# Performance work log

Measured on AMD Instinct MI355X. Metric: run time of the kernel, lower is better.

The kernel has to match this reference:

```python
import jax, jax.numpy as jnp
import numpy as np

B, R, L, F, H = 65536, 12, 16, 8, 64  # batch, rss_dim, n_leds, led_feat_dim, head_dim

def setup_inputs() -> dict:
    key = jax.random.key(0)
    ks = jax.random.split(key, 20)
    p = lambda k, shp, s=0.1: (jax.random.normal(k, shp, dtype=jnp.float32) * s)
    return {
        "rss_t": jax.random.uniform(ks[0], (B, R, 1), dtype=jnp.float32),
        "led_features": jax.random.normal(ks[1], (B, L, F), dtype=jnp.float32),
        "led_positions": jax.random.normal(ks[2], (B, L, 3), dtype=jnp.float32),
        "prev_pos": jax.random.normal(ks[3], (B, 3), dtype=jnp.float32),
        "freq_mask": jax.random.randint(ks[4], (R, L), 0, 2).astype(jnp.int32),
        # intensity_gate: Linear(1,16) -> ReLU -> Linear(16,1) -> Sigmoid
        "gw1": p(ks[5], (1, 16)), "gb1": p(ks[6], (16,)),
        "gw2": p(ks[7], (16, 1)), "gb2": p(ks[8], (1,)),
        # query_proj: Linear(1,32) -> ReLU -> Linear(32,64)
        "qw1": p(ks[9], (1, 32)), "qb1": p(ks[10], (32,)),
        "qw2": p(ks[11], (32, H)), "qb2": p(ks[12], (H,)),
        # key_proj: Linear(F+3,32) -> ReLU -> Linear(32,64)
        "kw1": p(ks[13], (F + 3, 32)), "kb1": p(ks[14], (32,)),
        "kw2": p(ks[15], (32, H)), "kb2": p(ks[16], (H,)),
        "sigma": jnp.float32(0.5),
    }

def reference(rss_t, led_features, led_positions, prev_pos, freq_mask,
              gw1, gb1, gw2, gb2, qw1, qb1, qw2, qb2, kw1, kb1, kw2, kb2, sigma):
    # intensity gate with hard threshold
    gate = jax.nn.sigmoid(jax.nn.relu(rss_t @ gw1 + gb1) @ gw2 + gb2)  # [B,R,1]
    iw = (rss_t > 0.5).astype(rss_t.dtype) * gate                      # [B,R,1]
    # query / key projections
    Q = jax.nn.relu((rss_t * iw) @ qw1 + qb1) @ qw2 + qb2              # [B,R,H]
    led_input = jnp.concatenate([led_features, led_positions], axis=-1)  # [B,L,F+3]
    K = jax.nn.relu(led_input @ kw1 + kb1) @ kw2 + kb2                 # [B,L,H]
    scores = jnp.einsum("brh,blh->brl", Q, K)                          # [B,R,L]
    # distance bias
    dist_sq = jnp.sum((prev_pos[:, None, :] - led_positions) ** 2, axis=-1)  # [B,L]
    scores = scores - dist_sq[:, None, :] / (2.0 * sigma ** 2)
    # mask + softmax
    neg = jnp.finfo(scores.dtype).min
    scores = jnp.where(freq_mask[None, :, :] == 0, neg, scores)
    attn = jax.nn.softmax(scores, axis=-1)                             # [B,R,L]
    return attn, iw.squeeze(-1)
```

## Files before the change

### kernel.cpp

```cpp
#include <hip/hip_runtime.h>

#define B_TOT 65536
#define R 12
#define L 16
#define NB 8
#define NEG_MIN -3.402823466e38f

#define WS_V   0
#define WS_C   32
#define WS_PM  40
#define WS_BP  64
#define WS_TAB 96
#define TROW   72
#define WS_WF  2472

#define WROWS (4 * 16 * 40 + 8)

typedef __attribute__((ext_vector_type(8))) short short8;
typedef __attribute__((ext_vector_type(4))) float f32x4;

static __device__ __forceinline__ short f2bf(float f) {
    uint32_t u = __float_as_uint(f);
    uint32_t r = u + 0x7FFFu + ((u >> 16) & 1u);
    return (short)(r >> 16);
}

static __device__ __forceinline__ unsigned cvt_pk_bf16(float a, float b) {
    unsigned d;
    asm("v_cvt_pk_bf16_f32 %0, %1, %2" : "=v"(d) : "v"(a), "v"(b));
    return d;
}

__global__ __launch_bounds__(256) void nfh_pre(
    const float* __restrict__ qw1, const float* __restrict__ qb1,
    const float* __restrict__ qw2, const float* __restrict__ qb2,
    const float* __restrict__ kw2, const float* __restrict__ kb2,
    const float* __restrict__ kw1, const float* __restrict__ kb1,
    const int*   __restrict__ fmask,
    float* __restrict__ ws)
{
    __shared__ float sM[1024];
    __shared__ float su[32];
    __shared__ float sw1[32], sb1[32], sbp[32], sbq[32];
    const int t = threadIdx.x;

    if (t < 32) { sw1[t] = qw1[t]; sb1[t] = qb1[t]; }
    for (int e = t; e < 1024; e += 256) {
        const int i = e >> 5, j = e & 31;
        float acc = 0.f;
        for (int h = 0; h < 64; ++h) acc = fmaf(qw2[i * 64 + h], kw2[j * 64 + h], acc);
        sM[e] = acc;
    }
    if (t < 32) {
        float au = 0.f, av = 0.f;
        for (int h = 0; h < 64; ++h) {
            au = fmaf(qw2[t * 64 + h], kb2[h], au);
            av = fmaf(kw2[t * 64 + h], qb2[h], av);
        }
        su[t] = au;
        ws[WS_V + t] = av;
        const float w = qw1[t];
        sbp[t] = (w != 0.f) ? (-qb1[t] / w) : 3.0e30f;
    }
    if (t == 64) {
        float acc = 0.f;
        for (int h = 0; h < 64; ++h) acc = fmaf(qb2[h], kb2[h], acc);
        ws[WS_C] = acc;
    }
    if (t < 12) {
        int pm = 0;
        for (int l = 0; l < 16; ++l) if (fmask[t * 16 + l] != 0) pm |= (1 << l);
        ((int*)ws)[WS_PM + t] = pm;
    }
    __syncthreads();
    if (t < 32) {
        const float key = sbp[t];
        int rank = 0;
        #pragma unroll
        for (int i = 0; i < 32; ++i) {
            const float vi = sbp[i];
            rank += (vi < key || (vi == key && i < t)) ? 1 : 0;
        }
        sbq[rank] = key;
    }
    __syncthreads();
    if (t < 32) ws[WS_BP + t] = sbq[t];

    for (int task = t; task < 33 * 32 + 33; task += 256) {
        const int m = (task < 33 * 32) ? (task >> 5) : (task - 33 * 32);
        const float xi = (m == 0) ? sbq[0] - 1.f
                       : ((m == 32) ? sbq[31] + 1.f
                                    : sbq[m - 1] + 0.5f * (sbq[m] - sbq[m - 1]));
        if (task < 33 * 32) {
            const int j = task & 31;
            float A = 0.f, Bv = 0.f;
            for (int i = 0; i < 32; ++i) {
                if (fmaf(sw1[i], xi, sb1[i]) > 0.f) {
                    A  = fmaf(sw1[i], sM[i * 32 + j], A);
                    Bv = fmaf(sb1[i], sM[i * 32 + j], Bv);
                }
            }
            ws[WS_TAB + m * TROW + j] = A;
            ws[WS_TAB + m * TROW + 36 + j] = Bv;
        } else {
            float Au = 0.f, Bu = 0.f;
            for (int i = 0; i < 32; ++i) {
                if (fmaf(sw1[i], xi, sb1[i]) > 0.f) {
                    Au = fmaf(sw1[i], su[i], Au);
                    Bu = fmaf(sb1[i], su[i], Bu);
                }
            }
            ws[WS_TAB + m * TROW + 32] = Au;
            ws[WS_TAB + m * TROW + 36 + 32] = Bu;
        }
    }

    {
        const int fr = t >> 6;
        const int li = t & 63;
        const int jl = li & 15, kb = li >> 4;
        const int T = fr & 1, term = fr >> 1;
        const int q = ((jl >> 2) << 3) + (T << 2) + (jl & 3);
        short* wsp = (short*)(ws + WS_WF);
        #pragma unroll
        for (int e = 0; e < 8; ++e) {
            const int k = kb * 8 + e;
            float w = 0.f;
            if (term == 0) {
                if (k < 11)       w = kw1[k * 32 + q];
                else if (k == 11) w = kb1[q];
            } else {
                if (k < 11)       w = kw1[k * 32 + q];
                else if (k == 11) { const float b = kb1[q];
                                    w = b - __uint_as_float(((uint32_t)(uint16_t)f2bf(b)) << 16); }
                else if (k < 23)  { const float a = kw1[(k - 12) * 32 + q];
                                    w = a - __uint_as_float(((uint32_t)(uint16_t)f2bf(a)) << 16); }
            }
            wsp[(fr * 64 + li) * 8 + e] = f2bf(w);
        }
    }
}

__global__ __launch_bounds__(128, 4) void nfh_main(
    const float* __restrict__ rss,
    const float* __restrict__ feat,
    const float* __restrict__ pos,
    const float* __restrict__ prev,
    const float* __restrict__ gw1, const float* __restrict__ gb1,
    const float* __restrict__ gw2, const float* __restrict__ gb2,
    const float* __restrict__ sigma_p,
    const float* __restrict__ ws,
    float* __restrict__ out)
{
    __shared__ short s_in[2 * WROWS];
    __shared__ short s_ttf[NB * 384];
    __shared__ float s_dq[NB * 16];
    __shared__ float s_tc[NB * 12];

    const int t = threadIdx.x;
    const int lane = t & 63;
    const int wv = t >> 6;
    const int lg = lane >> 4;
    const int b0 = blockIdx.x * NB;
    const float sigma = sigma_p[0];
    const float inv2s2 = 1.f / (2.f * sigma * sigma);

    const short* wsp = (const short*)(ws + WS_WF);
    const short8 wf0 = *(const short8*)(wsp + (0 * 64 + lane) * 8);
    const short8 wf1 = *(const short8*)(wsp + (1 * 64 + lane) * 8);
    const short8 wf2 = *(const short8*)(wsp + (2 * 64 + lane) * 8);
    const short8 wf3 = *(const short8*)(wsp + (3 * 64 + lane) * 8);
    const f32x4 v0 = *(const f32x4*)(ws + WS_V + lg * 8);
    const f32x4 v1 = *(const f32x4*)(ws + WS_V + lg * 8 + 4);
    const float cconst = ws[WS_C];

    if (lane < 8) s_in[wv * WROWS + 4 * 16 * 40 + lane] = 0;

    {
        const int bb1 = t >> 4, l1 = t & 15;
        const int b = b0 + bb1;
        float in[12];
        const float4* f4 = (const float4*)(feat + ((size_t)b * (L * 8) + l1 * 8));
        const float4 fa = f4[0], fb = f4[1];
        in[0] = fa.x; in[1] = fa.y; in[2] = fa.z; in[3] = fa.w;
        in[4] = fb.x; in[5] = fb.y; in[6] = fb.z; in[7] = fb.w;
        const float* pp = pos + ((size_t)b * (L * 3) + l1 * 3);
        in[8] = pp[0]; in[9] = pp[1]; in[10] = pp[2];
        in[11] = 1.0f;

        float dsq = 0.f;
        #pragma unroll
        for (int m = 0; m < 3; ++m) {
            const float d = prev[b * 3 + m] - in[8 + m];
            dsq = fmaf(d, d, dsq);
        }
        s_dq[bb1 * 16 + l1] = cconst - dsq * inv2s2;

        unsigned hp[6], lp[6];
        #pragma unroll
        for (int p = 0; p < 6; ++p) {
            const float a = in[2 * p], c = in[2 * p + 1];
            const unsigned h = cvt_pk_bf16(a, c);
            hp[p] = h;
            const float h0 = __uint_as_float(h << 16);
            const float h1 = __uint_as_float(h & 0xFFFF0000u);
            lp[p] = cvt_pk_bf16(a - h0, c - h1);
        }
        const unsigned lp5m = (lp[5] & 0xFFFFu) | 0x3F800000u;

        uint4* rowp = (uint4*)&s_in[wv * WROWS + ((bb1 & 3) * 16 + l1) * 40];
        rowp[0] = make_uint4(hp[0], hp[1], hp[2], hp[3]);
        rowp[1] = make_uint4(hp[4], hp[5], 0u, 0u);
        rowp[2] = make_uint4(lp[0], lp[1], lp[2], lp[3]);
        rowp[3] = make_uint4(lp[4], lp5m, hp[0], hp[1]);
        rowp[4] = make_uint4(hp[2], hp[3], hp[4], hp[5] & 0xFFFFu);
    }

    if ((t & 15) < R) {
        const int bb2 = t >> 4;
        const int r2 = t & 15;
        const int b = b0 + bb2;
        const float x = rss[(size_t)b * R + r2];
        float z = gb2[0];
        #pragma unroll
        for (int i = 0; i < 16; ++i) {
            const float h = fmaxf(fmaf(x, gw1[i], gb1[i]), 0.f);
            z = fmaf(h, gw2[i], z);
        }
        const float gate = 1.f / (1.f + __expf(-z));
        const float iw = (x > 0.5f) ? gate : 0.f;
        out[(size_t)B_TOT * R * L + (size_t)b * R + r2] = iw;
        const float xq = x * iw;

        int k = 0;
        #pragma unroll
        for (int m = 0; m < 32; ++m) k += (xq > ws[WS_BP + m]) ? 1 : 0;
        const float* row = ws + WS_TAB + k * TROW;
        const float4* ra = (const float4*)row;
        const float4* rb = (const float4*)(row + 36);
        s_tc[bb2 * 12 + r2] = fmaf(xq, row[32], row[68]);
        #pragma unroll
        for (int kb = 0; kb < 4; ++kb) {
            const float4 a0 = ra[kb * 2], c0 = rb[kb * 2];
            const float4 a1 = ra[kb * 2 + 1], c1 = rb[kb * 2 + 1];
            uint4 pk;
            pk.x = cvt_pk_bf16(fmaf(xq, a0.x, c0.x), fmaf(xq, a0.y, c0.y));
            pk.y = cvt_pk_bf16(fmaf(xq, a0.z, c0.z), fmaf(xq, a0.w, c0.w));
            pk.z = cvt_pk_bf16(fmaf(xq, a1.x, c1.x), fmaf(xq, a1.y, c1.y));
            pk.w = cvt_pk_bf16(fmaf(xq, a1.z, c1.z), fmaf(xq, a1.w, c1.w));
            *(uint4*)&s_ttf[bb2 * 384 + (kb * 12 + r2) * 8] = pk;
        }
    }

    asm volatile("s_waitcnt lgkmcnt(0)" ::: "memory");

    {
        const int r = lane & 15;
        const int pm = (r < R) ? ((const int*)ws)[WS_PM + r] : 0;

        #pragma unroll
        for (int i = 0; i < 4; ++i) {
            const int bb = wv * 4 + i;
            const short* rowb = &s_in[wv * WROWS + (i * 16 + r) * 40];
            const short8 i1 = *(const short8*)(rowb + lg * 8);
            const short8 i2 = *(const short8*)(rowb + 16 + lg * 8);

            f32x4 d0 = {0.f, 0.f, 0.f, 0.f};
            f32x4 d1 = {0.f, 0.f, 0.f, 0.f};
            d0 = __builtin_amdgcn_mfma_f32_16x16x32_bf16(wf0, i1, d0, 0, 0, 0);
            d0 = __builtin_amdgcn_mfma_f32_16x16x32_bf16(wf2, i2, d0, 0, 0, 0);
            d1 = __builtin_amdgcn_mfma_f32_16x16x32_bf16(wf1, i1, d1, 0, 0, 0);
            d1 = __builtin_amdgcn_mfma_f32_16x16x32_bf16(wf3, i2, d1, 0, 0, 0);

            float vbp = 0.f;
            #pragma unroll
            for (int j = 0; j < 4; ++j) {
                d0[j] = fmaxf(d0[j], 0.f);
                vbp = fmaf(v0[j], d0[j], vbp);
            }
            #pragma unroll
            for (int j = 0; j < 4; ++j) {
                d1[j] = fmaxf(d1[j], 0.f);
                vbp = fmaf(v1[j], d1[j], vbp);
            }
            vbp += __shfl_xor(vbp, 16);
            vbp += __shfl_xor(vbp, 32);
            const float vbl = vbp + s_dq[bb * 16 + r];

            uint4 afp;
            afp.x = cvt_pk_bf16(d0[0], d0[1]);
            afp.y = cvt_pk_bf16(d0[2], d0[3]);
            afp.z = cvt_pk_bf16(d1[0], d1[1]);
            afp.w = cvt_pk_bf16(d1[2], d1[3]);
            const short8 af = *(const short8*)&afp;

            short8 bf = (short8){0, 0, 0, 0, 0, 0, 0, 0};
            float tc = 0.f;
            if (r < R) {
                bf = *(const short8*)&s_ttf[bb * 384 + (lg * 12 + r) * 8];
                tc = s_tc[bb * 12 + r];
            }
            f32x4 acc = {0.f, 0.f, 0.f, 0.f};
            acc = __builtin_amdgcn_mfma_f32_16x16x32_bf16(af, bf, acc, 0, 0, 0);

            float sc[4];
            #pragma unroll
            for (int j = 0; j < 4; ++j) {
                const float vbj = __shfl(vbl, lg * 4 + j);
                sc[j] = acc[j] + tc + vbj;
                if (!((pm >> (lg * 4 + j)) & 1)) sc[j] = NEG_MIN;
            }
            float mx = fmaxf(fmaxf(sc[0], sc[1]), fmaxf(sc[2], sc[3]));
            mx = fmaxf(mx, __shfl_xor(mx, 16));
            mx = fmaxf(mx, __shfl_xor(mx, 32));
            float sum = 0.f;
            #pragma unroll
            for (int j = 0; j < 4; ++j) { sc[j] = __expf(sc[j] - mx); sum += sc[j]; }
            sum += __shfl_xor(sum, 16);
            sum += __shfl_xor(sum, 32);
            const float inv = 1.f / sum;

            if (r < R) {
                float4* op = (float4*)(out + ((size_t)(b0 + bb) * R + r) * L + lg * 4);
                *op = make_float4(sc[0] * inv, sc[1] * inv, sc[2] * inv, sc[3] * inv);
            }
        }
    }
}

extern "C" void kernel_launch(void* const* d_in, const int* in_sizes, int n_in,
                              void* d_out, int out_size, void* d_ws, size_t ws_size,
                              hipStream_t stream) {
    const float* rss   = (const float*)d_in[0];
    const float* feat  = (const float*)d_in[1];
    const float* pos   = (const float*)d_in[2];
    const float* prev  = (const float*)d_in[3];
    const int*   fmask = (const int*)d_in[4];
    const float* gw1   = (const float*)d_in[5];
    const float* gb1   = (const float*)d_in[6];
    const float* gw2   = (const float*)d_in[7];
    const float* gb2   = (const float*)d_in[8];
    const float* qw1   = (const float*)d_in[9];
    const float* qb1   = (const float*)d_in[10];
    const float* qw2   = (const float*)d_in[11];
    const float* qb2   = (const float*)d_in[12];
    const float* kw1   = (const float*)d_in[13];
    const float* kb1   = (const float*)d_in[14];
    const float* kw2   = (const float*)d_in[15];
    const float* kb2   = (const float*)d_in[16];
    const float* sigma = (const float*)d_in[17];
    float* out = (float*)d_out;
    float* ws  = (float*)d_ws;

    nfh_pre<<<1, 256, 0, stream>>>(qw1, qb1, qw2, qb2, kw2, kb2, kw1, kb1, fmask, ws);
    nfh_main<<<B_TOT / NB, 128, 0, stream>>>(
        rss, feat, pos, prev,
        gw1, gb1, gw2, gb2,
        sigma, ws, out);
}
```

Measured before the change: 172.0 us.

## Build query tables per lane via shuffles, drop shared staging, double block size

```diff
diff --git a/kernel.cpp b/kernel.cpp
--- a/kernel.cpp
+++ b/kernel.cpp
@@ -3,7 +3,7 @@
 #define B_TOT 65536
 #define R 12
 #define L 16
-#define NB 8
+#define NB 16
 #define NEG_MIN -3.402823466e38f
 
 #define WS_V   0
@@ -141,7 +141,7 @@
     }
 }
 
-__global__ __launch_bounds__(128, 4) void nfh_main(
+__global__ __launch_bounds__(256, 8) void nfh_main(
     const float* __restrict__ rss,
     const float* __restrict__ feat,
     const float* __restrict__ pos,
@@ -152,10 +152,7 @@
     const float* __restrict__ ws,
     float* __restrict__ out)
 {
-    __shared__ short s_in[2 * WROWS];
-    __shared__ short s_ttf[NB * 384];
-    __shared__ float s_dq[NB * 16];
-    __shared__ float s_tc[NB * 12];
+    __shared__ short s_in[4 * WROWS];
 
     const int t = threadIdx.x;
     const int lane = t & 63;
@@ -176,6 +173,7 @@
 
     if (lane < 8) s_in[wv * WROWS + 4 * 16 * 40 + lane] = 0;
 
+    float my_dq;
     {
         const int bb1 = t >> 4, l1 = t & 15;
         const int b = b0 + bb1;
@@ -194,7 +192,7 @@
             const float d = prev[b * 3 + m] - in[8 + m];
             dsq = fmaf(d, d, dsq);
         }
-        s_dq[bb1 * 16 + l1] = cconst - dsq * inv2s2;
+        my_dq = cconst - dsq * inv2s2;
 
         unsigned hp[6], lp[6];
         #pragma unroll
@@ -216,54 +214,50 @@
         rowp[4] = make_uint4(hp[2], hp[3], hp[4], hp[5] & 0xFFFFu);
     }
 
-    if ((t & 15) < R) {
+    float my_xq = 0.f;
+    {
         const int bb2 = t >> 4;
         const int r2 = t & 15;
-        const int b = b0 + bb2;
-        const float x = rss[(size_t)b * R + r2];
-        float z = gb2[0];
-        #pragma unroll
-        for (int i = 0; i < 16; ++i) {
-            const float h = fmaxf(fmaf(x, gw1[i], gb1[i]), 0.f);
-            z = fmaf(h, gw2[i], z);
-        }
-        const float gate = 1.f / (1.f + __expf(-z));
-        const float iw = (x > 0.5f) ? gate : 0.f;
-        out[(size_t)B_TOT * R * L + (size_t)b * R + r2] = iw;
-        const float xq = x * iw;
-
-        int k = 0;
-        #pragma unroll
-        for (int m = 0; m < 32; ++m) k += (xq > ws[WS_BP + m]) ? 1 : 0;
-        const float* row = ws + WS_TAB + k * TROW;
-        const float4* ra = (const float4*)row;
-        const float4* rb = (const float4*)(row + 36);
-        s_tc[bb2 * 12 + r2] = fmaf(xq, row[32], row[68]);
-        #pragma unroll
-        for (int kb = 0; kb < 4; ++kb) {
-            const float4 a0 = ra[kb * 2], c0 = rb[kb * 2];
-            const float4 a1 = ra[kb * 2 + 1], c1 = rb[kb * 2 + 1];
-            uint4 pk;
-            pk.x = cvt_pk_bf16(fmaf(xq, a0.x, c0.x), fmaf(xq, a0.y, c0.y));
-            pk.y = cvt_pk_bf16(fmaf(xq, a0.z, c0.z), fmaf(xq, a0.w, c0.w));
-            pk.z = cvt_pk_bf16(fmaf(xq, a1.x, c1.x), fmaf(xq, a1.y, c1.y));
-            pk.w = cvt_pk_bf16(fmaf(xq, a1.z, c1.z), fmaf(xq, a1.w, c1.w));
-            *(uint4*)&s_ttf[bb2 * 384 + (kb * 12 + r2) * 8] = pk;
-        }
-    }
+        if (r2 < R) {
+            const int b = b0 + bb2;
+            const float x = rss[(size_t)b * R + r2];
+            float z = gb2[0];
+            #pragma unroll
+            for (int i = 0; i < 16; ++i) {
+                const float h = fmaxf(fmaf(x, gw1[i], gb1[i]), 0.f);
+                z = fmaf(h, gw2[i], z);
+            }
+            const float gate = 1.f / (1.f + __expf(-z));
+            const float iw = (x > 0.5f) ? gate : 0.f;
+            out[(size_t)B_TOT * R * L + (size_t)b * R + r2] = iw;
+            my_xq = x * iw;
+        }
+    }
+    int my_k = 0;
+    #pragma unroll
+    for (int m = 0; m < 32; ++m) my_k += (my_xq > ws[WS_BP + m]) ? 1 : 0;
+    const float* myrow = ws + WS_TAB + my_k * TROW;
+    const float my_tc = fmaf(my_xq, myrow[32], myrow[68]);
 
     asm volatile("s_waitcnt lgkmcnt(0)" ::: "memory");
 
     {
         const int r = lane & 15;
         const int pm = (r < R) ? ((const int*)ws)[WS_PM + r] : 0;
-
-        #pragma unroll
+        const int j0 = lg * 8;
+
+        #pragma unroll 1
         for (int i = 0; i < 4; ++i) {
             const int bb = wv * 4 + i;
+            const int src = i * 16 + r;
+            const float xq_s = __shfl(my_xq, src);
+            const int   k_s  = __shfl(my_k,  src);
+            const float tc_s = __shfl(my_tc, src);
+            const float dq_s = __shfl(my_dq, src);
+
             const short* rowb = &s_in[wv * WROWS + (i * 16 + r) * 40];
-            const short8 i1 = *(const short8*)(rowb + lg * 8);
-            const short8 i2 = *(const short8*)(rowb + 16 + lg * 8);
+            const short8 i1 = *(const short8*)(rowb + j0);
+            const short8 i2 = *(const short8*)(rowb + 16 + j0);
 
             f32x4 d0 = {0.f, 0.f, 0.f, 0.f};
             f32x4 d1 = {0.f, 0.f, 0.f, 0.f};
@@ -285,7 +279,7 @@
             }
             vbp += __shfl_xor(vbp, 16);
             vbp += __shfl_xor(vbp, 32);
-            const float vbl = vbp + s_dq[bb * 16 + r];
+            const float vbl = vbp + dq_s;
 
             uint4 afp;
             afp.x = cvt_pk_bf16(d0[0], d0[1]);
@@ -294,12 +288,18 @@
             afp.w = cvt_pk_bf16(d1[2], d1[3]);
             const short8 af = *(const short8*)&afp;
 
-            short8 bf = (short8){0, 0, 0, 0, 0, 0, 0, 0};
-            float tc = 0.f;
-            if (r < R) {
-                bf = *(const short8*)&s_ttf[bb * 384 + (lg * 12 + r) * 8];
-                tc = s_tc[bb * 12 + r];
-            }
+            const float* rowt = ws + WS_TAB + k_s * TROW;
+            const float4 a0 = *(const float4*)(rowt + j0);
+            const float4 a1 = *(const float4*)(rowt + j0 + 4);
+            const float4 c0 = *(const float4*)(rowt + 36 + j0);
+            const float4 c1 = *(const float4*)(rowt + 36 + j0 + 4);
+            uint4 bfp;
+            bfp.x = cvt_pk_bf16(fmaf(xq_s, a0.x, c0.x), fmaf(xq_s, a0.y, c0.y));
+            bfp.y = cvt_pk_bf16(fmaf(xq_s, a0.z, c0.z), fmaf(xq_s, a0.w, c0.w));
+            bfp.z = cvt_pk_bf16(fmaf(xq_s, a1.x, c1.x), fmaf(xq_s, a1.y, c1.y));
+            bfp.w = cvt_pk_bf16(fmaf(xq_s, a1.z, c1.z), fmaf(xq_s, a1.w, c1.w));
+            const short8 bf = *(const short8*)&bfp;
+
             f32x4 acc = {0.f, 0.f, 0.f, 0.f};
             acc = __builtin_amdgcn_mfma_f32_16x16x32_bf16(af, bf, acc, 0, 0, 0);
 
@@ -307,7 +307,7 @@
             #pragma unroll
             for (int j = 0; j < 4; ++j) {
                 const float vbj = __shfl(vbl, lg * 4 + j);
-                sc[j] = acc[j] + tc + vbj;
+                sc[j] = acc[j] + tc_s + vbj;
                 if (!((pm >> (lg * 4 + j)) & 1)) sc[j] = NEG_MIN;
             }
             float mx = fmaxf(fmaxf(sc[0], sc[1]), fmaxf(sc[2], sc[3]));
@@ -353,7 +353,7 @@
     float* ws  = (float*)d_ws;
 
     nfh_pre<<<1, 256, 0, stream>>>(qw1, qb1, qw2, qb2, kw2, kb2, kw1, kb1, fmask, ws);
-    nfh_main<<<B_TOT / NB, 128, 0, stream>>>(
+    nfh_main<<<B_TOT / NB, 256, 0, stream>>>(
         rss, feat, pos, prev,
         gw1, gb1, gw2, gb2,
         sigma, ws, out);
```

New measurement: 162.3 us. 5.7% less time.
